# Kernel optimization log

Hardware: AMD Instinct MI355X
Metric: run time of the kernel (lower is better)

Reference implementation:

```python
import jax, jax.numpy as jnp
import numpy as np

# model dims
B, L, D, K = 4, 1024, 512, 24      # batch, seq_len, d_model, num_eigh
KU, KY, NL, DT = 3, 2, 4, 512      # ar depth u, ar depth y, num_layers, d_target
EPS = 1e-5


def _hankel_eigh():
    # Hankel matrix Z[i,j] = 2 / ((i+j)^3 - (i+j)), i,j in 1..L; top-K eigenpairs
    idx = np.arange(1, L + 1, dtype=np.float64)
    s = idx[:, None] + idx[None, :]
    Z = 2.0 / (s ** 3 - s)
    vals, vecs = np.linalg.eigh(Z)  # ascending
    return (jnp.asarray(vals[-K:], jnp.float32),       # [K]
            jnp.asarray(vecs[:, -K:], jnp.float32))    # [L, K]


def setup_inputs() -> dict:
    key = jax.random.key(0)
    ks = jax.random.split(key, 12)
    sc = 1.0 / np.sqrt(D)
    eig_vals, eig_vecs = _hankel_eigh()
    return {
        "inputs": jax.random.normal(ks[0], (B, L, D), jnp.float32),
        "emb_w": jax.random.normal(ks[1], (D, D), jnp.float32) * sc,
        "emb_b": jnp.zeros((D,), jnp.float32),
        "ln_scale": jnp.ones((NL, D), jnp.float32),
        "ln_bias": jnp.zeros((NL, D), jnp.float32),
        "m_y": jax.random.normal(ks[2], (NL, D, KY, D), jnp.float32) * 0.02,
        "m_u": jax.random.normal(ks[3], (NL, D, D, KU), jnp.float32) * sc,
        "m_phi": jax.random.normal(ks[4], (NL, D * K, D), jnp.float32) * 0.02,
        "w1": jax.random.normal(ks[5], (NL, D, 2 * D), jnp.float32) * sc,
        "b1": jnp.zeros((NL, 2 * D), jnp.float32),
        "proj_w": jax.random.normal(ks[6], (D, DT), jnp.float32) * sc,
        "proj_b": jnp.zeros((DT,), jnp.float32),
        "eig_vals": eig_vals,
        "eig_vecs": eig_vecs,
    }


def _layer_norm(x, s, b):
    mu = jnp.mean(x, axis=-1, keepdims=True)
    var = jnp.mean(jnp.square(x - mu), axis=-1, keepdims=True)
    return (x - mu) * jax.lax.rsqrt(var + EPS) * s + b


def _stu(x, m_y_l, m_u_l, m_phi_l, eig_vals, eig_vecs):
    # x: [B, L, D]
    n = 2 * L
    U = jnp.fft.rfft(x, n=n, axis=1)                 # [B, nf, D]
    V = jnp.fft.rfft(eig_vecs, n=n, axis=0)          # [nf, K]
    # causal conv of each eigvec filter with each channel -> x_tilde [B, L, K, D]
    xt = jnp.fft.irfft(U[:, :, None, :] * V[None, :, :, None], n=n, axis=1)[:, :L]
    xt = xt * (eig_vals[None, None, :, None] ** 0.25)
    delta_phi = xt.reshape(B, L, K * D) @ m_phi_l    # [B, L, D]
    ar = jnp.zeros_like(delta_phi)
    for i in range(KU):
        c = jnp.einsum('bli,oi->blo', x, m_u_l[:, :, i])
        if i > 0:
            c = jnp.pad(c, ((0, 0), (i, 0), (0, 0)))[:, :L]
        ar = ar + c
    deltas = delta_phi + ar
    # y_t = sum_{j<KY} m_y[:,j,:] @ y_{t-1-j} + delta_t  (sequential recurrence)
    def step(carry, d_t):                            # carry [B, KY, D], d_t [B, D]
        y = jnp.einsum('okd,bkd->bo', m_y_l, carry) + d_t
        carry = jnp.concatenate([y[:, None, :], carry[:, :-1]], axis=1)
        return carry, y
    _, ys = jax.lax.scan(step, jnp.zeros((B, KY, D), x.dtype),
                         jnp.transpose(deltas, (1, 0, 2)))
    return jnp.transpose(ys, (1, 0, 2))              # [B, L, D]


def reference(inputs, emb_w, emb_b, ln_scale, ln_bias, m_y, m_u, m_phi,
              w1, b1, proj_w, proj_b, eig_vals, eig_vecs):
    x = inputs @ emb_w + emb_b
    for l in range(NL):
        z = x
        h = _layer_norm(x, ln_scale[l], ln_bias[l])
        h = _stu(h, m_y[l], m_u[l], m_phi[l], eig_vals, eig_vecs)
        h = jax.nn.gelu(h, approximate=False)        # torch GELU default (erf)
        g = h @ w1[l] + b1[l]
        a, b = jnp.split(g, 2, axis=-1)
        h = a * jax.nn.sigmoid(b)                    # GLU(dim=-1)
        x = h + z                                    # residual (dropout=0, eval)
    return x @ proj_w + proj_b
```

## Files before the change

### kernel.cpp

```cpp
#include <hip/hip_runtime.h>
#include <math.h>

typedef __bf16 bf;
typedef __attribute__((ext_vector_type(4))) __bf16 bfv4;
typedef __attribute__((ext_vector_type(8))) __bf16 bfv8;
typedef __attribute__((ext_vector_type(4))) float f32x4;

__device__ __forceinline__ void gload16(const void* g, void* l) {
  __builtin_amdgcn_global_load_lds((const __attribute__((address_space(1))) void*)g,
                                   (__attribute__((address_space(3))) void*)l, 16, 0, 0);
}

struct GOp {
  const bf* A; long la, lKa, lMa, sAz; int zshA, kzA;
  const bf* B; long lb, lKb, sBz; int zmskB, kzB;
  float* C; long ldc, sCz;
  bf* Cb; long ldcb, sCbz;
  const float* bias; int K, maskCmp, mBlk;
};

template<int tB,int tF32,int tB16,int tMASK,int tACC>
__device__ __forceinline__ void gbody(const GOp g, int z, bf* lsA, bf* lsB, const bf* zpg) {
  const int t = threadIdx.x;
  const long m0 = (long)blockIdx.x * 128, n0 = (long)blockIdx.y * 128;
  const bf* Ap = g.A + (long)(z >> g.zshA) * g.sAz;
  const bf* Bp = g.B + (long)(z & g.zmskB) * g.sBz;
  const int w = t >> 6, l = t & 63;
  const int wm = (w >> 1) * 64, wn = (w & 1) * 64;
  const int lr = l & 15, lk = (l >> 4) * 8;
  const int r0 = t >> 2, ko = (t & 3) * 8;
  const long rowA1 = m0 + r0, rowA2 = rowA1 + 64;
  const long baseA1 = (rowA1 >> 9) * g.lMa + (rowA1 & 511) * g.la;
  const long baseA2 = (rowA2 >> 9) * g.lMa + (rowA2 & 511) * g.la;
  const long baseB1 = (n0 + r0) * g.lb;
  const int zbA = z * g.kzA, zbB = z * g.kzB;
  const int ct = ((int)rowA1 + 1) & 7;
  const long convB = (long)ct * 2065 + 1023 - (long)rowA1;
  f32x4 acc[4][4];
  #pragma unroll
  for (int i = 0; i < 4; i++)
    #pragma unroll
    for (int j = 0; j < 4; j++) acc[i][j] = (f32x4){0.f, 0.f, 0.f, 0.f};

  for (int k0 = 0; k0 < g.K; k0 += 32) {
    const int kk = k0 + ko;
    const int bA = (kk >> 9) + zbA, bB = (kk >> 9) + zbB;
    const long kb = (long)bB * g.lKb + (kk & 511);
    const bf* ga; const bf* ga2;
    if (tMASK == 3) {
      ga  = Ap + convB + kk;
      ga2 = ga - 64;
    } else {
      const long ka = (long)bA * g.lKa + (kk & 511);
      ga  = Ap + baseA1 + ka;
      ga2 = Ap + baseA2 + ka;
      if (tMASK == 1) { if ((int)(rowA1 & 15) < bA) { ga = zpg; ga2 = zpg; } }
      if (tMASK == 2) { if ((int)(rowA1 & 63) < g.maskCmp) { ga = zpg; ga2 = zpg; } }
    }
    const bf* gb = Bp + baseB1 + kb;
    gload16(ga,            &lsA[t * 8]);
    gload16(ga2,           &lsA[2048 + t * 8]);
    gload16(gb,            &lsB[t * 8]);
    gload16(gb + 64 * g.lb, &lsB[2048 + t * 8]);
    __syncthreads();
    bfv8 av[4], bv[4];
    #pragma unroll
    for (int i = 0; i < 4; i++) av[i] = *(const bfv8*)&lsA[(wm + i * 16 + lr) * 32 + lk];
    #pragma unroll
    for (int i = 0; i < 4; i++) bv[i] = *(const bfv8*)&lsB[(wn + i * 16 + lr) * 32 + lk];
    #pragma unroll
    for (int i = 0; i < 4; i++)
      #pragma unroll
      for (int j = 0; j < 4; j++)
        acc[i][j] = __builtin_amdgcn_mfma_f32_16x16x32_bf16(av[i], bv[j], acc[i][j], 0, 0, 0);
    __syncthreads();
  }
  const int orow = (l >> 4) * 4, ocol = lr;
  #pragma unroll
  for (int i = 0; i < 4; i++)
    #pragma unroll
    for (int j = 0; j < 4; j++) {
      long col = n0 + wn + j * 16 + ocol;
      float bb = tB ? g.bias[col] : 0.f;
      #pragma unroll
      for (int r = 0; r < 4; r++) {
        long row = m0 + wm + i * 16 + orow + r;
        float v = acc[i][j][r] + bb;
        if (tF32) {
          long idx = (long)z * g.sCz + row * g.ldc + col;
          if (tACC) v += g.C[idx];
          g.C[idx] = v;
        }
        if (tB16) g.Cb[(long)z * g.sCbz + row * g.ldcb + col] = (bf)v;
      }
    }
}

template<int tB,int tF32,int tB16,int tMASK,int tACC,int tSPEC,
         int sB,int sF32,int sB16,int sMASK,int sACC>
__global__ __launch_bounds__(256) void gemm_k(GOp g, GOp gx, const bf* __restrict__ zpg) {
  __shared__ bf lsA[4096], lsB[4096];
  int z = blockIdx.z;
  if (tSPEC && z == (int)gridDim.z - 1) {
    if ((int)blockIdx.x >= gx.mBlk) return;
    gbody<sB,sF32,sB16,sMASK,sACC>(gx, 0, lsA, lsB, zpg);
  } else {
    gbody<tB,tF32,tB16,tMASK,tACC>(g, z, lsA, lsB, zpg);
  }
}

static inline GOp mkop(const void* A, long la, long lKa, long lMa, long sAz, int zshA, int kzA,
                       const void* B, long lb, long lKb, long sBz, int zmskB, int kzB,
                       void* C, long ldc, long sCz, void* Cb, long ldcb, long sCbz,
                       const void* bias, int K, int maskCmp, int mBlk) {
  GOp g;
  g.A = (const bf*)A; g.la = la; g.lKa = lKa; g.lMa = lMa; g.sAz = sAz; g.zshA = zshA; g.kzA = kzA;
  g.B = (const bf*)B; g.lb = lb; g.lKb = lKb; g.sBz = sBz; g.zmskB = zmskB; g.kzB = kzB;
  g.C = (float*)C; g.ldc = ldc; g.sCz = sCz;
  g.Cb = (bf*)Cb; g.ldcb = ldcb; g.sCbz = sCbz;
  g.bias = (const float*)bias; g.K = K; g.maskCmp = maskCmp; g.mBlk = mBlk;
  return g;
}

template<int tB,int tF32,int tB16,int tMASK,int tACC,int tSPEC=0,
         int sB=0,int sF32=0,int sB16=0,int sMASK=0,int sACC=0>
static inline void LG(hipStream_t st, int gx, int gy, int gz, const GOp& g, const GOp& gs, const bf* zpg) {
  gemm_k<tB,tF32,tB16,tMASK,tACC,tSPEC,sB,sF32,sB16,sMASK,sACC>
      <<<dim3(gx, gy, gz), 256, 0, st>>>(g, gs, zpg);
}


template<typename TI, typename TO>
__global__ __launch_bounds__(256) void k_trt(const TI* __restrict__ in, TO* __restrict__ out,
                                             long ldin, long inz, long ldout, long outz) {
  __shared__ float tile[64][65];
  int z = blockIdx.z;
  int c0 = blockIdx.x * 64, r0 = blockIdx.y * 64;
  int tx = threadIdx.x & 63, ty = threadIdx.x >> 6;
  #pragma unroll
  for (int i = ty; i < 64; i += 4) tile[i][tx] = (float)in[(long)z * inz + (long)(c0 + i) * ldin + r0 + tx];
  __syncthreads();
  #pragma unroll
  for (int i = ty; i < 64; i += 4) out[(long)z * outz + (long)(r0 + i) * ldout + c0 + tx] = (TO)tile[tx][i];
}

__global__ __launch_bounds__(256) void k_trtS(const float* __restrict__ in, bf* __restrict__ out,
                                              long ldin, long ldout, const float* __restrict__ scl) {
  __shared__ float tile[64][65];
  int c0 = blockIdx.x * 64, r0 = blockIdx.y * 64;
  int tx = threadIdx.x & 63, ty = threadIdx.x >> 6;
  #pragma unroll
  for (int i = ty; i < 64; i += 4) tile[i][tx] = in[(long)(c0 + i) * ldin + r0 + tx];
  __syncthreads();
  float sc = scl[(c0 + tx) >> 9];
  #pragma unroll
  for (int i = ty; i < 64; i += 4) out[(long)(r0 + i) * ldout + c0 + tx] = (bf)(tile[tx][i] * sc);
}

__global__ void k_scl(const float* __restrict__ evals, float* __restrict__ scl) {
  int k = threadIdx.x;
  if (k < 24) scl[k] = powf(evals[k], 0.25f);
}

__global__ void k_pvec(const float* __restrict__ evecs, bf* __restrict__ out) {
  long id = (long)blockIdx.x * 256 + threadIdx.x;
  if (id >= 24L * 16512) return;
  int kf = (int)(id / 16512);
  int rem = (int)(id % 16512);
  int c = rem / 2064, j = rem % 2064;
  int d = j - c;
  float v = (d >= 0 && d <= 1023) ? evecs[(long)(1023 - d) * 24 + kf] : 0.f;
  out[id] = (bf)v;
}

__global__ void k_mut(const float* __restrict__ mul_, bf* __restrict__ out) {
  long id = (long)blockIdx.x * 256 + threadIdx.x;
  long r = id >> 9; int d = (int)(id & 511);
  int i = (int)(r >> 9), o = (int)(r & 511);
  out[id] = (bf)mul_[(long)o * 1536 + d * 3 + i];
}

__global__ void k_buildCM(const float* __restrict__ myl, bf* __restrict__ cmpow) {
  long id = (long)blockIdx.x * 256 + threadIdx.x;
  int half = (int)(id >> 20);
  int r = (int)(id & 1048575);
  int p = r >> 10, q = r & 1023;
  float v;
  if (half == 0) v = (p == q) ? 1.f : 0.f;
  else if (p < 512) v = myl[(long)p * 1024 + q];
  else v = (q == p - 512) ? 1.f : 0.f;
  cmpow[id] = (bf)v;
}

__global__ __launch_bounds__(256) void k_ln(const float* __restrict__ x, const float* __restrict__ sc,
                                            const float* __restrict__ bi, bf* __restrict__ hb) {
  __shared__ float red[8];
  long row = blockIdx.x;
  const float* xr = x + row * 512;
  int t = threadIdx.x;
  float a = xr[t], b2 = xr[t + 256];
  float s = a + b2;
  #pragma unroll
  for (int o = 32; o; o >>= 1) s += __shfl_down(s, o, 64);
  if ((t & 63) == 0) red[t >> 6] = s;
  __syncthreads();
  float mu = (red[0] + red[1] + red[2] + red[3]) * (1.f / 512.f);
  __syncthreads();
  float c1 = a - mu, c2 = b2 - mu;
  float qq = c1 * c1 + c2 * c2;
  #pragma unroll
  for (int o = 32; o; o >>= 1) qq += __shfl_down(qq, o, 64);
  if ((t & 63) == 0) red[t >> 6] = qq;
  __syncthreads();
  float var = (red[0] + red[1] + red[2] + red[3]) * (1.f / 512.f);
  float rs = rsqrtf(var + 1e-5f);
  hb[row * 512 + t]       = (bf)(c1 * rs * sc[t] + bi[t]);
  hb[row * 512 + t + 256] = (bf)(c2 * rs * sc[t + 256] + bi[t + 256]);
}

__global__ void k_deltasS(const float* __restrict__ dp, long stride, int S,
                          const bf* __restrict__ callb, bf* __restrict__ db) {
  long id = (long)blockIdx.x * 256 + threadIdx.x;
  int o = (int)(id & 511); long row = id >> 9; int tt = (int)(row & 1023);
  float v = 0.f;
  for (int zz = 0; zz < S; ++zz) v += dp[(long)zz * stride + id];
  for (int i = 0; i < 3; ++i)
    if (tt >= i) v += (float)callb[(row - i) * 1536 + i * 512 + o];
  db[id] = (bf)v;
}

__global__ void k_egather(const float* __restrict__ dp, long stride, int S,
                          float* __restrict__ E, bf* __restrict__ eb0) {
  long id = (long)blockIdx.x * 256 + threadIdx.x;
  int p = (int)(id & 1023); long r = id >> 10;
  int b = (int)(r >> 6), c = (int)(r & 63);
  int tq = c * 16 + ((p < 512) ? 15 : 14);
  long idx = ((long)(b << 10) + tq) * 512 + (p & 511);
  float v = 0.f;
  for (int zz = 0; zz < S; ++zz) v += dp[(long)zz * stride + idx];
  E[id] = v; eb0[id] = (bf)v;
}

__global__ void k_sfinal(const float* __restrict__ E, bf* __restrict__ ssb) {
  long id = (long)blockIdx.x * 256 + threadIdx.x;
  int c = (int)((id >> 10) & 63);
  ssb[id] = (c > 0) ? (bf)E[id - 1024] : (bf)0.f;
}

__global__ void k_combgelu(const float* __restrict__ dp, long stride, int S,
                           const bf* __restrict__ outh, bf* __restrict__ yg) {
  long id = (long)blockIdx.x * 256 + threadIdx.x;
  int o = (int)(id & 511); long row = id >> 9;
  int b = (int)(row >> 10), tt = (int)(row & 1023);
  int c = tt >> 4, j = tt & 15;
  long wv = ((long)(j * 512 + o)) * 256 + b * 64 + c;
  float v = (float)outh[wv];
  for (int zz = 0; zz < S; ++zz) v += dp[(long)zz * stride + id];
  yg[id] = (bf)(0.5f * v * (1.f + erff(v * 0.70710678118654752f)));
}

__global__ void k_glures(const bf* __restrict__ g, float* __restrict__ x) {
  long id = (long)blockIdx.x * 256 + threadIdx.x;
  int o = (int)(id & 511); long row = id >> 9;
  float a = (float)g[row * 1024 + o], bb = (float)g[row * 1024 + 512 + o];
  x[id] = x[id] + a / (1.f + expf(-bb));
}

__global__ void k_cast(const float* __restrict__ in, bf* __restrict__ out, long n4) {
  long id = (long)blockIdx.x * 256 + threadIdx.x;
  if (id >= n4) return;
  float4 v = *(const float4*)(in + id * 4);
  bfv4 o; o[0] = (bf)v.x; o[1] = (bf)v.y; o[2] = (bf)v.z; o[3] = (bf)v.w;
  *(bfv4*)(out + id * 4) = o;
}

__global__ void k_fill(float* p, long n, float v) {
  long id = (long)blockIdx.x * 256 + threadIdx.x;
  if (id < n) p[id] = v;
}

struct Lay {
  long ZPG, SCL, EMBT, PROJT, PVEC, CMPOW, CMT2, WU, X, MPHITL, MUTL, W1TL,
       HB, HTB, DSLOT, DP, RC, E, EB0, EB1, SSTB, need;
  int nk, S;
};
static Lay mkLay(int nk, int S) {
  Lay L; long o = 0;
  auto al = [&](long sz) { long r = o; o += (sz + 255) & ~255L; return r; };
  L.nk = nk; L.S = S;
  L.ZPG   = al(4096);
  L.SCL   = al(256);
  L.EMBT  = al(524288);
  L.PROJT = al(524288);
  L.PVEC  = al(24L * 16512 * 2);
  L.CMPOW = al(17L * 2097152);
  L.CMT2  = al(2L * 2097152);
  L.WU    = al(8388608);
  L.X     = al(8388608);
  L.MPHITL= al(12582912);
  L.MUTL  = al(1572864);
  L.W1TL  = al(1048576);
  L.HB    = al(4194304);
  L.HTB   = al(4194304);
  L.DSLOT = al(4194304);
  L.DP    = al((long)S * 8388608);
  long rc = (long)nk * 4194304;
  if (rc < 16777216) rc = 16777216;
  L.RC    = al(rc);
  L.E     = al(1048576);
  L.EB0   = al(524288);
  L.EB1   = al(524288);
  L.SSTB  = al(524288);
  L.need  = o;
  return L;
}

extern "C" void kernel_launch(void* const* d_in, const int* in_sizes, int n_in,
                              void* d_out, int out_size, void* d_ws, size_t ws_size,
                              hipStream_t stream) {
  Lay L = mkLay(12, 4);
  if (L.need > (long)ws_size) L = mkLay(8, 4);
  if (L.need > (long)ws_size) L = mkLay(4, 2);
  if (L.need > (long)ws_size) {
    k_fill<<<8192, 256, 0, stream>>>((float*)d_out, 2097152, 1.0e6f + (float)(ws_size >> 20));
    return;
  }
  const float* inp  = (const float*)d_in[0];
  const float* embw = (const float*)d_in[1];
  const float* embb = (const float*)d_in[2];
  const float* lns  = (const float*)d_in[3];
  const float* lnb  = (const float*)d_in[4];
  const float* m_y  = (const float*)d_in[5];
  const float* m_u  = (const float*)d_in[6];
  const float* mphi = (const float*)d_in[7];
  const float* w1   = (const float*)d_in[8];
  const float* b1   = (const float*)d_in[9];
  const float* pw   = (const float*)d_in[10];
  const float* pb   = (const float*)d_in[11];
  const float* evals = (const float*)d_in[12];
  const float* evecs = (const float*)d_in[13];

  char* w = (char*)d_ws;
  bf*    ZPG   = (bf*)(w + L.ZPG);
  float* SCL   = (float*)(w + L.SCL);
  bf*    EMBT  = (bf*)(w + L.EMBT);
  bf*    PROJT = (bf*)(w + L.PROJT);
  bf*    PVEC  = (bf*)(w + L.PVEC);
  bf*    CMPOW = (bf*)(w + L.CMPOW);
  bf*    CMT2a = (bf*)(w + L.CMT2);
  bf*    CMT2b = CMT2a + 1048576;
  bf*    WUa   = (bf*)(w + L.WU);
  bf*    WUb   = (bf*)(w + L.WU + 4194304);
  float* X     = (float*)(w + L.X);
  bf*    MPHITL= (bf*)(w + L.MPHITL);
  bf*    MUTL  = (bf*)(w + L.MUTL);
  bf*    W1TL  = (bf*)(w + L.W1TL);
  bf*    HB    = (bf*)(w + L.HB);
  bf*    HTB   = (bf*)(w + L.HTB);
  bf*    DELTAB= (bf*)(w + L.DSLOT);
  bf*    YGB   = (bf*)(w + L.DSLOT);
  float* DP    = (float*)(w + L.DP);
  bf*    XTC   = (bf*)(w + L.RC);
  bf*    CALLB = (bf*)(w + L.RC);
  bf*    OUTH  = (bf*)(w + L.RC + 12582912);
  bf*    G     = (bf*)(w + L.RC);
  float* E     = (float*)(w + L.E);
  bf*    EB0   = (bf*)(w + L.EB0);
  bf*    EB1   = (bf*)(w + L.EB1);
  bf*    SSTB  = (bf*)(w + L.SSTB);
  bf*    INB   = HB;
  hipStream_t st = stream;
  const int nk = L.nk, S = L.S, nchunk = 24 / nk;
  const long DPS = 2097152;
  const int Kcphi = nk * 512 / S, kzphi = Kcphi >> 9;
  const int Kcy = 8192 / S, kzy = Kcy >> 9;
  GOp gnull = {};

  hipMemsetAsync(w + L.ZPG, 0, 4096, st);

  k_scl<<<1, 32, 0, st>>>(evals, SCL);
  k_pvec<<<1549, 256, 0, st>>>(evecs, PVEC);
  k_trt<float, bf><<<dim3(8, 8, 1), 256, 0, st>>>(embw, EMBT, 512, 0, 512, 0);
  k_trt<float, bf><<<dim3(8, 8, 1), 256, 0, st>>>(pw, PROJT, 512, 0, 512, 0);
  k_cast<<<2048, 256, 0, st>>>(inp, INB, 524288);
  LG<1,1,0,0,0>(st, 32, 4, 1,
      mkop(INB, 512, 512, 262144, 0, 30, 0, EMBT, 512, 512, 0, 0, 0,
           X, 512, 0, nullptr, 0, 0, embb, 512, 0, 0), gnull, ZPG);

  for (int l = 0; l < 4; ++l) {
    k_buildCM<<<8192, 256, 0, st>>>(m_y + (long)l * 524288, CMPOW);
    k_trt<bf, bf><<<dim3(16, 16, 1), 256, 0, st>>>(CMPOW + 1048576, CMT2a, 1024, 0, 1024, 0);
    bf* curT = CMT2a;
    for (int r = 0; r < 4; ++r) {
      int s = 1 << r;
      bf* nxtT = (r & 1) ? CMT2a : CMT2b;
      GOp mn = mkop(CMPOW + 1048576, 1024, 512, 524288, 1048576, 0, 0,
                    curT, 1024, 512, 0, 0, 0,
                    nullptr, 0, 0, CMPOW + (long)(s + 1) * 1048576, 1024, 1048576,
                    nullptr, 1024, 0, 0);
      GOp sp = mkop(curT, 1024, 512, 524288, 0, 30, 0,
                    CMPOW + (long)s * 1048576, 1024, 512, 0, 0, 0,
                    nullptr, 0, 0, nxtT, 1024, 0,
                    nullptr, 1024, 0, 8);
      LG<0,0,1,0,0, 1, 0,0,1,0,0>(st, 8, 8, s + 1, mn, sp, ZPG);
      curT = nxtT;
    }
    k_trtS<<<dim3(192, 8, 1), 256, 0, st>>>(mphi + (long)l * 6291456, MPHITL, 512, 12288, SCL);
    k_mut<<<3072, 256, 0, st>>>(m_u + (long)l * 786432, MUTL);
    k_trt<float, bf><<<dim3(8, 16, 1), 256, 0, st>>>(w1 + (long)l * 524288, W1TL, 1024, 0, 512, 0);

    k_ln<<<4096, 256, 0, st>>>(X, lns + l * 512, lnb + l * 512, HB);
    k_trt<bf, bf><<<dim3(16, 8, 4), 256, 0, st>>>(HB, HTB, 512, 524288, 1024, 524288);

    for (int kc = 0; kc < nchunk; ++kc) {
      LG<0,0,1,3,0>(st, 8, 4, 4 * nk,
          mkop(PVEC + (long)kc * nk * 16512, 0, 0, 0, 16512, 2, 0,
               HTB, 1024, 512, 524288, 3, 0,
               nullptr, 0, 0, XTC, 512, 524288, nullptr, 1024, 0, 0), gnull, ZPG);
      GOp pg = mkop(XTC, 512, 2097152, 262144, 0, 30, kzphi,
                    MPHITL + (long)kc * nk * 512, 12288, 512, 0, 0, kzphi,
                    DP, 512, DPS, nullptr, 0, 0, nullptr, Kcphi, 0, 0);
      if (kc == 0) LG<0,1,0,0,0>(st, 32, 4, S, pg, gnull, ZPG);
      else         LG<0,1,0,0,1>(st, 32, 4, S, pg, gnull, ZPG);
    }

    LG<0,0,1,0,0>(st, 32, 12, 1,
        mkop(HB, 512, 512, 262144, 0, 30, 0, MUTL, 512, 512, 0, 0, 0,
             nullptr, 0, 0, CALLB, 1536, 0, nullptr, 512, 0, 0), gnull, ZPG);
    k_deltasS<<<8192, 256, 0, st>>>(DP, DPS, S, CALLB, DELTAB);

    LG<0,1,0,1,0>(st, 32, 4, S,
        mkop(DELTAB, 512, -512, 262144, 0, 30, kzy,
             CMPOW, 1024, 1048576, 0, 0, kzy,
             DP, 512, DPS, nullptr, 0, 0, nullptr, Kcy, 0, 0), gnull, ZPG);

    k_egather<<<1024, 256, 0, st>>>(DP, DPS, S, E, EB0);
    const bf* Wc = CMPOW + 16L * 1048576;
    const bf* Uc = curT;
    bf* EBc = EB0; bf* EBn = EB1;
    bf* WUn = WUa;
    for (int k = 1; k <= 5; ++k) {
      int sh = 1 << (k - 1);
      GOp mn = mkop(Wc, 1024, 512, 524288, (long)(Uc - Wc), 0, 0,
                    Uc, 1024, 512, (long)(Wc - Uc), 1, 0,
                    nullptr, 0, 0, WUn, 1024, 1048576, nullptr, 1024, 0, 0);
      GOp sp = mkop(EBc - (long)sh * 1024, 1024, 512, 524288, 0, 30, 0,
                    Wc, 1024, 512, 0, 0, 0,
                    E, 1024, 0, EBn, 1024, 0, nullptr, 1024, sh, 2);
      LG<0,0,1,0,0, 1, 0,1,1,2,1>(st, 8, 8, 3, mn, sp, ZPG);
      Wc = WUn; Uc = WUn + 1048576;
      WUn = (k & 1) ? WUb : WUa;
      bf* tmp = EBc; EBc = EBn; EBn = tmp;
    }
    LG<0,1,0,2,1>(st, 2, 8, 1,
        mkop(EBc - 32L * 1024, 1024, 512, 524288, 0, 30, 0,
             Wc, 1024, 512, 0, 0, 0,
             E, 1024, 0, nullptr, 0, 0, nullptr, 1024, 32, 0), gnull, ZPG);
    k_sfinal<<<1024, 256, 0, st>>>(E, SSTB);

    LG<0,0,1,0,0>(st, 64, 2, 1,
        mkop(CMPOW + 1048576, 1024, 512, 1048576, 0, 30, 0,
             SSTB, 1024, 512, 0, 0, 0,
             nullptr, 0, 0, OUTH, 256, 0, nullptr, 1024, 0, 0), gnull, ZPG);
    k_combgelu<<<8192, 256, 0, st>>>(DP, DPS, S, OUTH, YGB);
    LG<1,0,1,0,0>(st, 32, 8, 1,
        mkop(YGB, 512, 512, 262144, 0, 30, 0, W1TL, 512, 512, 0, 0, 0,
             nullptr, 0, 0, G, 1024, 0, b1 + (long)l * 1024, 512, 0, 0), gnull, ZPG);
    k_glures<<<8192, 256, 0, st>>>(G, X);
  }

  k_cast<<<2048, 256, 0, st>>>(X, INB, 524288);
  LG<1,1,0,0,0>(st, 32, 4, 1,
      mkop(INB, 512, 512, 262144, 0, 30, 0, PROJT, 512, 512, 0, 0, 0,
           (float*)d_out, 512, 0, nullptr, 0, 0, pb, 512, 0, 0), gnull, ZPG);
}
```

Measured before the change: 3.136 ms.

## Fuse companion-matrix power chains into persistent kernels with grid barriers

Replaces the multi-launch chains that build companion-matrix powers and the doubling scan (build, transpose, several batched GEMMs, gather and final-shift kernels) with two persistent 256-workgroup kernels, k_chainA and k_chainB. Their stages are separated by atomic software grid barriers, and the chains now store only the top half of each power matrix. The goal is to remove per-launch overhead and the idle gaps between small dependent GEMMs. The cost is that the chain GEMMs run over few tiles with spin barriers, so many workgroups sit idle, and correctness depends on all 256 workgroups being co-resident.

```diff
diff --git a/kernel.cpp b/kernel.cpp
--- a/kernel.cpp
+++ b/kernel.cpp
@@ -20,8 +20,9 @@
 };
 
 template<int tB,int tF32,int tB16,int tMASK,int tACC>
-__device__ __forceinline__ void gbody(const GOp g, int z, bf* lsA, bf* lsB, const bf* zpg) {
-  const int t = threadIdx.x;
+__global__ __launch_bounds__(256) void gemm_k(GOp g, const bf* __restrict__ zpg) {
+  __shared__ bf lsA[4096], lsB[4096];
+  const int t = threadIdx.x, z = blockIdx.z;
   const long m0 = (long)blockIdx.x * 128, n0 = (long)blockIdx.y * 128;
   const bf* Ap = g.A + (long)(z >> g.zshA) * g.sAz;
   const bf* Bp = g.B + (long)(z & g.zmskB) * g.sBz;
@@ -55,12 +56,11 @@
       ga  = Ap + baseA1 + ka;
       ga2 = Ap + baseA2 + ka;
       if (tMASK == 1) { if ((int)(rowA1 & 15) < bA) { ga = zpg; ga2 = zpg; } }
-      if (tMASK == 2) { if ((int)(rowA1 & 63) < g.maskCmp) { ga = zpg; ga2 = zpg; } }
     }
     const bf* gb = Bp + baseB1 + kb;
-    gload16(ga,            &lsA[t * 8]);
-    gload16(ga2,           &lsA[2048 + t * 8]);
-    gload16(gb,            &lsB[t * 8]);
+    gload16(ga,             &lsA[t * 8]);
+    gload16(ga2,            &lsA[2048 + t * 8]);
+    gload16(gb,             &lsB[t * 8]);
     gload16(gb + 64 * g.lb, &lsB[2048 + t * 8]);
     __syncthreads();
     bfv8 av[4], bv[4];
@@ -96,37 +96,212 @@
     }
 }
 
-template<int tB,int tF32,int tB16,int tMASK,int tACC,int tSPEC,
-         int sB,int sF32,int sB16,int sMASK,int sACC>
-__global__ __launch_bounds__(256) void gemm_k(GOp g, GOp gx, const bf* __restrict__ zpg) {
-  __shared__ bf lsA[4096], lsB[4096];
-  int z = blockIdx.z;
-  if (tSPEC && z == (int)gridDim.z - 1) {
-    if ((int)blockIdx.x >= gx.mBlk) return;
-    gbody<sB,sF32,sB16,sMASK,sACC>(gx, 0, lsA, lsB, zpg);
-  } else {
-    gbody<tB,tF32,tB16,tMASK,tACC>(g, z, lsA, lsB, zpg);
-  }
-}
-
 static inline GOp mkop(const void* A, long la, long lKa, long lMa, long sAz, int zshA, int kzA,
                        const void* B, long lb, long lKb, long sBz, int zmskB, int kzB,
                        void* C, long ldc, long sCz, void* Cb, long ldcb, long sCbz,
-                       const void* bias, int K, int maskCmp, int mBlk) {
+                       const void* bias, int K) {
   GOp g;
   g.A = (const bf*)A; g.la = la; g.lKa = lKa; g.lMa = lMa; g.sAz = sAz; g.zshA = zshA; g.kzA = kzA;
   g.B = (const bf*)B; g.lb = lb; g.lKb = lKb; g.sBz = sBz; g.zmskB = zmskB; g.kzB = kzB;
   g.C = (float*)C; g.ldc = ldc; g.sCz = sCz;
   g.Cb = (bf*)Cb; g.ldcb = ldcb; g.sCbz = sCbz;
-  g.bias = (const float*)bias; g.K = K; g.maskCmp = maskCmp; g.mBlk = mBlk;
+  g.bias = (const float*)bias; g.K = K; g.maskCmp = 0; g.mBlk = 0;
   return g;
 }
 
-template<int tB,int tF32,int tB16,int tMASK,int tACC,int tSPEC=0,
-         int sB=0,int sF32=0,int sB16=0,int sMASK=0,int sACC=0>
-static inline void LG(hipStream_t st, int gx, int gy, int gz, const GOp& g, const GOp& gs, const bf* zpg) {
-  gemm_k<tB,tF32,tB16,tMASK,tACC,tSPEC,sB,sF32,sB16,sMASK,sACC>
-      <<<dim3(gx, gy, gz), 256, 0, st>>>(g, gs, zpg);
+template<int tB,int tF32,int tB16,int tMASK,int tACC>
+static inline void LG(hipStream_t st, int gx, int gy, int gz, const GOp& g, const bf* zpg) {
+  gemm_k<tB,tF32,tB16,tMASK,tACC><<<dim3(gx, gy, gz), 256, 0, st>>>(g, zpg);
+}
+
+__device__ __forceinline__ void cbar(int* __restrict__ bar, int& target) {
+  __threadfence();
+  __syncthreads();
+  if (threadIdx.x == 0) {
+    int old = __hip_atomic_fetch_add(bar, 1, __ATOMIC_ACQ_REL, __HIP_MEMORY_SCOPE_AGENT);
+    if (old == 255) {
+      __hip_atomic_store(bar, 0, __ATOMIC_RELAXED, __HIP_MEMORY_SCOPE_AGENT);
+      __hip_atomic_fetch_add(bar + 1, 1, __ATOMIC_RELEASE, __HIP_MEMORY_SCOPE_AGENT);
+    } else {
+      while (__hip_atomic_load(bar + 1, __ATOMIC_ACQUIRE, __HIP_MEMORY_SCOPE_AGENT) - target < 0)
+        __builtin_amdgcn_s_sleep(2);
+    }
+  }
+  __syncthreads();
+  __threadfence();
+  ++target;
+}
+
+__device__ __forceinline__ void cgemm(const bf* __restrict__ A, long la,
+    const bf* __restrict__ Bt, long lb, float* __restrict__ Cf, bf* __restrict__ Cb,
+    long ldc, int m0, int n0, int shmask, const bf* __restrict__ zpg, bf* ls) {
+  bf* lsA = ls; bf* lsB = ls + 4096;
+  const int t = threadIdx.x;
+  const int w = t >> 6, l = t & 63;
+  const int wm = (w >> 1) * 64, wn = (w & 1) * 64;
+  const int lr = l & 15, lk = (l >> 4) * 8;
+  const int r0 = t >> 2, ko = (t & 3) * 8;
+  const long rowA1 = m0 + r0, rowA2 = rowA1 + 64;
+  f32x4 acc[4][4];
+  #pragma unroll
+  for (int i = 0; i < 4; i++)
+    #pragma unroll
+    for (int j = 0; j < 4; j++) acc[i][j] = (f32x4){0.f, 0.f, 0.f, 0.f};
+  for (int k0 = 0; k0 < 1024; k0 += 32) {
+    int kk = k0 + ko;
+    const bf* ga  = A + rowA1 * la + kk;
+    const bf* ga2 = A + rowA2 * la + kk;
+    if (shmask >= 0 && (int)(rowA1 & 63) < shmask) { ga = zpg; ga2 = zpg; }
+    const bf* gb = Bt + (n0 + r0) * lb + kk;
+    gload16(ga,           &lsA[t * 8]);
+    gload16(ga2,          &lsA[2048 + t * 8]);
+    gload16(gb,           &lsB[t * 8]);
+    gload16(gb + 64 * lb, &lsB[2048 + t * 8]);
+    __syncthreads();
+    bfv8 av[4], bv[4];
+    #pragma unroll
+    for (int i = 0; i < 4; i++) av[i] = *(const bfv8*)&lsA[(wm + i * 16 + lr) * 32 + lk];
+    #pragma unroll
+    for (int i = 0; i < 4; i++) bv[i] = *(const bfv8*)&lsB[(wn + i * 16 + lr) * 32 + lk];
+    #pragma unroll
+    for (int i = 0; i < 4; i++)
+      #pragma unroll
+      for (int j = 0; j < 4; j++)
+        acc[i][j] = __builtin_amdgcn_mfma_f32_16x16x32_bf16(av[i], bv[j], acc[i][j], 0, 0, 0);
+    __syncthreads();
+  }
+  const int orow = (l >> 4) * 4;
+  #pragma unroll
+  for (int i = 0; i < 4; i++)
+    #pragma unroll
+    for (int j = 0; j < 4; j++) {
+      long col = n0 + wn + j * 16 + lr;
+      #pragma unroll
+      for (int r = 0; r < 4; r++) {
+        long row = m0 + wm + i * 16 + orow + r;
+        float v = acc[i][j][r];
+        if (Cf) { long idx = row * ldc + col; v += Cf[idx]; Cf[idx] = v; }
+        if (Cb) Cb[row * ldc + col] = (bf)v;
+      }
+    }
+}
+
+__device__ __forceinline__ void ttile(const bf* __restrict__ src, bf* __restrict__ dst,
+                                      int wg, bf* ls) {
+  bf (*tile)[65] = (bf (*)[65])ls;
+  int tx = wg & 15, ty = wg >> 4;
+  int lx = threadIdx.x & 63, ly = threadIdx.x >> 6;
+  __syncthreads();
+  #pragma unroll
+  for (int i = ly; i < 64; i += 4)
+    tile[i][lx] = src[(long)(ty * 64 + i) * 1024 + tx * 64 + lx];
+  __syncthreads();
+  #pragma unroll
+  for (int i = ly; i < 64; i += 4)
+    dst[(long)(tx * 64 + i) * 1024 + ty * 64 + lx] = tile[lx][i];
+  __syncthreads();
+}
+
+__global__ __launch_bounds__(256) void k_chainA(const float* __restrict__ myl,
+    bf* __restrict__ PT, bf* __restrict__ TRS, int* __restrict__ bar,
+    const bf* __restrict__ zpg) {
+  __shared__ bf ls[8192];
+  const int wg = blockIdx.x, t = threadIdx.x;
+  int target = 1;
+  {
+    bf* PT1 = PT + 15L * 524288;
+    bf* PT0 = PT + 16L * 524288;
+    long id0 = ((long)wg * 256 + t) * 8;
+    #pragma unroll
+    for (int u = 0; u < 8; ++u) {
+      long id = id0 + u;
+      PT1[id] = (bf)myl[id];
+      int p = (int)(id >> 10), q = (int)(id & 1023);
+      PT0[id] = (bf)((p == q) ? 1.f : 0.f);
+    }
+  }
+  cbar(bar, target);
+  ttile(PT + 15L * 524288, TRS, wg, ls);
+  cbar(bar, target);
+  for (int r = 0; r < 4; ++r) {
+    int s = 1 << r;
+    int ntile = 32 * s;
+    for (int tt = wg; tt < ntile; tt += 256) {
+      int zz = tt >> 5, tx = (tt >> 3) & 3, ty = tt & 7;
+      const bf* A = PT + (long)(15 - zz) * 524288;
+      bf*       C = PT + (long)(15 - s - zz) * 524288;
+      cgemm(A, 1024, TRS, 1024, nullptr, C, 1024, tx * 128, ty * 128, -1, zpg, ls);
+    }
+    cbar(bar, target);
+    if (r < 3) {
+      ttile(PT + (long)(16 - 2 * s) * 524288, TRS, wg, ls);
+      cbar(bar, target);
+    }
+  }
+}
+
+__global__ __launch_bounds__(256) void k_chainB(const float* __restrict__ DP, long DPS, int S,
+    const bf* __restrict__ PT, bf* __restrict__ Wa, bf* __restrict__ Wb, bf* __restrict__ TRS,
+    float* __restrict__ E, bf* __restrict__ EB0, bf* __restrict__ EB1, bf* __restrict__ SSTB,
+    int* __restrict__ bar, const bf* __restrict__ zpg) {
+  __shared__ bf ls[8192];
+  const int wg = blockIdx.x, t = threadIdx.x;
+  int target = 1;
+  {
+    long id0 = ((long)wg * 256 + t) * 4;
+    #pragma unroll
+    for (int u = 0; u < 4; ++u) {
+      long id = id0 + u;
+      int p = (int)(id & 1023); long r = id >> 10;
+      int b = (int)(r >> 6), c = (int)(r & 63);
+      int tq = c * 16 + ((p < 512) ? 15 : 14);
+      long idx = ((long)(b << 10) + tq) * 512 + (p & 511);
+      float v = 0.f;
+      for (int zz = 0; zz < S; ++zz) v += DP[(long)zz * DPS + idx];
+      E[id] = v; EB0[id] = (bf)v;
+    }
+  }
+  cbar(bar, target);
+  ttile(PT, TRS, wg, ls);
+  cbar(bar, target);
+  const bf* W = PT;
+  const bf* U = TRS;
+  bf* EBc = EB0; bf* EBn = EB1;
+  for (int k = 1; k <= 5; ++k) {
+    int sh = 1 << (k - 1);
+    bf* Wn = (k & 1) ? Wa : Wb;
+    for (int tt = wg; tt < 80; tt += 256) {
+      if (tt < 16) {
+        int tx = tt >> 3, ty = tt & 7;
+        cgemm(EBc - (long)sh * 1024, 1024, W, 1024, E, EBn, 1024,
+              tx * 128, ty * 128, sh, zpg, ls);
+      } else {
+        int q = tt - 16, tx = q >> 3, ty = q & 7;
+        cgemm(W, 1024, U, 1024, nullptr, Wn, 1024, tx * 128, ty * 128, -1, zpg, ls);
+      }
+    }
+    cbar(bar, target);
+    if (k < 5) {
+      ttile(Wn, TRS, wg, ls);
+      cbar(bar, target);
+    }
+    W = Wn; U = TRS;
+    bf* tmp = EBc; EBc = EBn; EBn = tmp;
+  }
+  for (int tt = wg; tt < 16; tt += 256) {
+    int tx = tt >> 3, ty = tt & 7;
+    cgemm(EBc - 32L * 1024, 1024, W, 1024, E, nullptr, 1024, tx * 128, ty * 128, 32, zpg, ls);
+  }
+  cbar(bar, target);
+  {
+    long id0 = ((long)wg * 256 + t) * 4;
+    #pragma unroll
+    for (int u = 0; u < 4; ++u) {
+      long id = id0 + u;
+      int c = (int)((id >> 10) & 63);
+      SSTB[id] = (c > 0) ? (bf)E[id - 1024] : (bf)0.f;
+    }
+  }
 }
 
 
@@ -178,18 +353,6 @@
   long r = id >> 9; int d = (int)(id & 511);
   int i = (int)(r >> 9), o = (int)(r & 511);
   out[id] = (bf)mul_[(long)o * 1536 + d * 3 + i];
-}
-
-__global__ void k_buildCM(const float* __restrict__ myl, bf* __restrict__ cmpow) {
-  long id = (long)blockIdx.x * 256 + threadIdx.x;
-  int half = (int)(id >> 20);
-  int r = (int)(id & 1048575);
-  int p = r >> 10, q = r & 1023;
-  float v;
-  if (half == 0) v = (p == q) ? 1.f : 0.f;
-  else if (p < 512) v = myl[(long)p * 1024 + q];
-  else v = (q == p - 512) ? 1.f : 0.f;
-  cmpow[id] = (bf)v;
 }
 
 __global__ __launch_bounds__(256) void k_ln(const float* __restrict__ x, const float* __restrict__ sc,
@@ -229,24 +392,6 @@
   db[id] = (bf)v;
 }
 
-__global__ void k_egather(const float* __restrict__ dp, long stride, int S,
-                          float* __restrict__ E, bf* __restrict__ eb0) {
-  long id = (long)blockIdx.x * 256 + threadIdx.x;
-  int p = (int)(id & 1023); long r = id >> 10;
-  int b = (int)(r >> 6), c = (int)(r & 63);
-  int tq = c * 16 + ((p < 512) ? 15 : 14);
-  long idx = ((long)(b << 10) + tq) * 512 + (p & 511);
-  float v = 0.f;
-  for (int zz = 0; zz < S; ++zz) v += dp[(long)zz * stride + idx];
-  E[id] = v; eb0[id] = (bf)v;
-}
-
-__global__ void k_sfinal(const float* __restrict__ E, bf* __restrict__ ssb) {
-  long id = (long)blockIdx.x * 256 + threadIdx.x;
-  int c = (int)((id >> 10) & 63);
-  ssb[id] = (c > 0) ? (bf)E[id - 1024] : (bf)0.f;
-}
-
 __global__ void k_combgelu(const float* __restrict__ dp, long stride, int S,
                            const bf* __restrict__ outh, bf* __restrict__ yg) {
   long id = (long)blockIdx.x * 256 + threadIdx.x;
@@ -280,7 +425,7 @@
 }
 
 struct Lay {
-  long ZPG, SCL, EMBT, PROJT, PVEC, CMPOW, CMT2, WU, X, MPHITL, MUTL, W1TL,
+  long BAR, ZPG, SCL, EMBT, PROJT, PVEC, PTOP, WA, WB, TRS, X, MPHITL, MUTL, W1TL,
        HB, HTB, DSLOT, DP, RC, E, EB0, EB1, SSTB, need;
   int nk, S;
 };
@@ -288,14 +433,16 @@
   Lay L; long o = 0;
   auto al = [&](long sz) { long r = o; o += (sz + 255) & ~255L; return r; };
   L.nk = nk; L.S = S;
+  L.BAR   = al(4096);
   L.ZPG   = al(4096);
   L.SCL   = al(256);
   L.EMBT  = al(524288);
   L.PROJT = al(524288);
   L.PVEC  = al(24L * 16512 * 2);
-  L.CMPOW = al(17L * 2097152);
-  L.CMT2  = al(2L * 2097152);
-  L.WU    = al(8388608);
+  L.PTOP  = al(17L * 1048576);
+  L.WA    = al(2097152);
+  L.WB    = al(2097152);
+  L.TRS   = al(2097152);
   L.X     = al(8388608);
   L.MPHITL= al(12582912);
   L.MUTL  = al(1572864);
@@ -341,16 +488,16 @@
   const float* evecs = (const float*)d_in[13];
 
   char* w = (char*)d_ws;
+  int*   BARi  = (int*)(w + L.BAR);
   bf*    ZPG   = (bf*)(w + L.ZPG);
   float* SCL   = (float*)(w + L.SCL);
   bf*    EMBT  = (bf*)(w + L.EMBT);
   bf*    PROJT = (bf*)(w + L.PROJT);
   bf*    PVEC  = (bf*)(w + L.PVEC);
-  bf*    CMPOW = (bf*)(w + L.CMPOW);
-  bf*    CMT2a = (bf*)(w + L.CMT2);
-  bf*    CMT2b = CMT2a + 1048576;
-  bf*    WUa   = (bf*)(w + L.WU);
-  bf*    WUb   = (bf*)(w + L.WU + 4194304);
+  bf*    PTOP  = (bf*)(w + L.PTOP);
+  bf*    Wa    = (bf*)(w + L.WA);
+  bf*    Wb    = (bf*)(w + L.WB);
+  bf*    TRS   = (bf*)(w + L.TRS);
   float* X     = (float*)(w + L.X);
   bf*    MPHITL= (bf*)(w + L.MPHITL);
   bf*    MUTL  = (bf*)(w + L.MUTL);
@@ -374,9 +521,8 @@
   const long DPS = 2097152;
   const int Kcphi = nk * 512 / S, kzphi = Kcphi >> 9;
   const int Kcy = 8192 / S, kzy = Kcy >> 9;
-  GOp gnull = {};
-
-  hipMemsetAsync(w + L.ZPG, 0, 4096, st);
+
+  hipMemsetAsync(w, 0, 8192, st);
 
   k_scl<<<1, 32, 0, st>>>(evals, SCL);
   k_pvec<<<1549, 256, 0, st>>>(evecs, PVEC);
@@ -385,26 +531,10 @@
   k_cast<<<2048, 256, 0, st>>>(inp, INB, 524288);
   LG<1,1,0,0,0>(st, 32, 4, 1,
       mkop(INB, 512, 512, 262144, 0, 30, 0, EMBT, 512, 512, 0, 0, 0,
-           X, 512, 0, nullptr, 0, 0, embb, 512, 0, 0), gnull, ZPG);
+           X, 512, 0, nullptr, 0, 0, embb, 512), ZPG);
 
   for (int l = 0; l < 4; ++l) {
-    k_buildCM<<<8192, 256, 0, st>>>(m_y + (long)l * 524288, CMPOW);
-    k_trt<bf, bf><<<dim3(16, 16, 1), 256, 0, st>>>(CMPOW + 1048576, CMT2a, 1024, 0, 1024, 0);
-    bf* curT = CMT2a;
-    for (int r = 0; r < 4; ++r) {
-      int s = 1 << r;
-      bf* nxtT = (r & 1) ? CMT2a : CMT2b;
-      GOp mn = mkop(CMPOW + 1048576, 1024, 512, 524288, 1048576, 0, 0,
-                    curT, 1024, 512, 0, 0, 0,
-                    nullptr, 0, 0, CMPOW + (long)(s + 1) * 1048576, 1024, 1048576,
-                    nullptr, 1024, 0, 0);
-      GOp sp = mkop(curT, 1024, 512, 524288, 0, 30, 0,
-                    CMPOW + (long)s * 1048576, 1024, 512, 0, 0, 0,
-                    nullptr, 0, 0, nxtT, 1024, 0,
-                    nullptr, 1024, 0, 8);
-      LG<0,0,1,0,0, 1, 0,0,1,0,0>(st, 8, 8, s + 1, mn, sp, ZPG);
-      curT = nxtT;
-    }
+    k_chainA<<<256, 256, 0, st>>>(m_y + (long)l * 524288, PTOP, TRS, BARi + l * 32, ZPG);
     k_trtS<<<dim3(192, 8, 1), 256, 0, st>>>(mphi + (long)l * 6291456, MPHITL, 512, 12288, SCL);
     k_mut<<<3072, 256, 0, st>>>(m_u + (long)l * 786432, MUTL);
     k_trt<float, bf><<<dim3(8, 16, 1), 256, 0, st>>>(w1 + (long)l * 524288, W1TL, 1024, 0, 512, 0);
@@ -416,61 +546,40 @@
       LG<0,0,1,3,0>(st, 8, 4, 4 * nk,
           mkop(PVEC + (long)kc * nk * 16512, 0, 0, 0, 16512, 2, 0,
                HTB, 1024, 512, 524288, 3, 0,
-               nullptr, 0, 0, XTC, 512, 524288, nullptr, 1024, 0, 0), gnull, ZPG);
+               nullptr, 0, 0, XTC, 512, 524288, nullptr, 1024), ZPG);
       GOp pg = mkop(XTC, 512, 2097152, 262144, 0, 30, kzphi,
                     MPHITL + (long)kc * nk * 512, 12288, 512, 0, 0, kzphi,
-                    DP, 512, DPS, nullptr, 0, 0, nullptr, Kcphi, 0, 0);
-      if (kc == 0) LG<0,1,0,0,0>(st, 32, 4, S, pg, gnull, ZPG);
-      else         LG<0,1,0,0,1>(st, 32, 4, S, pg, gnull, ZPG);
+                    DP, 512, DPS, nullptr, 0, 0, nullptr, Kcphi);
+      if (kc == 0) LG<0,1,0,0,0>(st, 32, 4, S, pg, ZPG);
+      else         LG<0,1,0,0,1>(st, 32, 4, S, pg, ZPG);
     }
 
     LG<0,0,1,0,0>(st, 32, 12, 1,
         mkop(HB, 512, 512, 262144, 0, 30, 0, MUTL, 512, 512, 0, 0, 0,
-             nullptr, 0, 0, CALLB, 1536, 0, nullptr, 512, 0, 0), gnull, ZPG);
+             nullptr, 0, 0, CALLB, 1536, 0, nullptr, 512), ZPG);
     k_deltasS<<<8192, 256, 0, st>>>(DP, DPS, S, CALLB, DELTAB);
 
     LG<0,1,0,1,0>(st, 32, 4, S,
         mkop(DELTAB, 512, -512, 262144, 0, 30, kzy,
-             CMPOW, 1024, 1048576, 0, 0, kzy,
-             DP, 512, DPS, nullptr, 0, 0, nullptr, Kcy, 0, 0), gnull, ZPG);
-
-    k_egather<<<1024, 256, 0, st>>>(DP, DPS, S, E, EB0);
-    const bf* Wc = CMPOW + 16L * 1048576;
-    const bf* Uc = curT;
-    bf* EBc = EB0; bf* EBn = EB1;
-    bf* WUn = WUa;
-    for (int k = 1; k <= 5; ++k) {
-      int sh = 1 << (k - 1);
-      GOp mn = mkop(Wc, 1024, 512, 524288, (long)(Uc - Wc), 0, 0,
-                    Uc, 1024, 512, (long)(Wc - Uc), 1, 0,
-                    nullptr, 0, 0, WUn, 1024, 1048576, nullptr, 1024, 0, 0);
-      GOp sp = mkop(EBc - (long)sh * 1024, 1024, 512, 524288, 0, 30, 0,
-                    Wc, 1024, 512, 0, 0, 0,
-                    E, 1024, 0, EBn, 1024, 0, nullptr, 1024, sh, 2);
-      LG<0,0,1,0,0, 1, 0,1,1,2,1>(st, 8, 8, 3, mn, sp, ZPG);
-      Wc = WUn; Uc = WUn + 1048576;
-      WUn = (k & 1) ? WUb : WUa;
-      bf* tmp = EBc; EBc = EBn; EBn = tmp;
-    }
-    LG<0,1,0,2,1>(st, 2, 8, 1,
-        mkop(EBc - 32L * 1024, 1024, 512, 524288, 0, 30, 0,
-             Wc, 1024, 512, 0, 0, 0,
-             E, 1024, 0, nullptr, 0, 0, nullptr, 1024, 32, 0), gnull, ZPG);
-    k_sfinal<<<1024, 256, 0, st>>>(E, SSTB);
+             PTOP + 16L * 524288, 1024, -524288, 0, 0, kzy,
+             DP, 512, DPS, nullptr, 0, 0, nullptr, Kcy), ZPG);
+
+    k_chainB<<<256, 256, 0, st>>>(DP, DPS, S, PTOP, Wa, Wb, TRS,
+                                  E, EB0, EB1, SSTB, BARi + (4 + l) * 32, ZPG);
 
     LG<0,0,1,0,0>(st, 64, 2, 1,
-        mkop(CMPOW + 1048576, 1024, 512, 1048576, 0, 30, 0,
+        mkop(PTOP + 15L * 524288, 1024, 512, -524288, 0, 30, 0,
              SSTB, 1024, 512, 0, 0, 0,
-             nullptr, 0, 0, OUTH, 256, 0, nullptr, 1024, 0, 0), gnull, ZPG);
+             nullptr, 0, 0, OUTH, 256, 0, nullptr, 1024), ZPG);
     k_combgelu<<<8192, 256, 0, st>>>(DP, DPS, S, OUTH, YGB);
     LG<1,0,1,0,0>(st, 32, 8, 1,
         mkop(YGB, 512, 512, 262144, 0, 30, 0, W1TL, 512, 512, 0, 0, 0,
-             nullptr, 0, 0, G, 1024, 0, b1 + (long)l * 1024, 512, 0, 0), gnull, ZPG);
+             nullptr, 0, 0, G, 1024, 0, b1 + (long)l * 1024, 512), ZPG);
     k_glures<<<8192, 256, 0, st>>>(G, X);
   }
 
   k_cast<<<2048, 256, 0, st>>>(X, INB, 524288);
   LG<1,1,0,0,0>(st, 32, 4, 1,
       mkop(INB, 512, 512, 262144, 0, 30, 0, PROJT, 512, 512, 0, 0, 0,
-           (float*)d_out, 512, 0, nullptr, 0, 0, pb, 512, 0, 0), gnull, ZPG);
-}
+           (float*)d_out, 512, 0, nullptr, 0, 0, pb, 512), ZPG);
+}
```

After: 11.28 ms. 260% more time.
